# Kernel tuning notes

Hardware: AMD Instinct MI355X
Metric: run time of the kernel (lower is better)

Reference implementation:

```python
import jax, jax.numpy as jnp
import numpy as np

D = 128      # d_feat / d_model
L = 512      # seq_len
H = 8        # heads (hardcoded in FourierBlock weights)
E = D // H   # head dim = 16
MODES = 64   # low-frequency modes (mode_select='low' -> index = range(MODES))
MA = 25      # moving_avg kernel
NL = 2       # e_layers
DFF = 512
EPS = 1e-5


def _positional(length, dim):
    pos = jnp.arange(length, dtype=jnp.float32)[:, None]
    div = jnp.exp(jnp.arange(0, dim, 2, dtype=jnp.float32) * (-np.log(10000.0) / dim))
    pe = jnp.zeros((length, dim), dtype=jnp.float32)
    pe = pe.at[:, 0::2].set(jnp.sin(pos * div))
    pe = pe.at[:, 1::2].set(jnp.cos(pos * div))
    return pe


def _mov_mean(x, k):
    # series_decomp moving average: replicate-pad (k-1)//2 each side, window mean stride 1
    pad = (k - 1) // 2
    xp = jnp.concatenate([jnp.repeat(x[:, :1], pad, axis=1), x,
                          jnp.repeat(x[:, -1:], pad, axis=1)], axis=1)
    cs = jnp.cumsum(xp, axis=1)
    cs = jnp.concatenate([jnp.zeros_like(cs[:, :1]), cs], axis=1)
    return (cs[:, k:] - cs[:, :-k]) / k


def _fourier_layer(x, Wq, bq, Wo, bo, fwr, fwi):
    # AutoCorrelationLayer(query proj -> FourierBlock -> out proj); k/v projections are unused by FourierBlock
    B = x.shape[0]
    q = (x @ Wq + bq).reshape(B, L, H, E).transpose(0, 2, 3, 1)   # B,H,E,L
    xft = jnp.fft.rfft(q, axis=-1)                                # B,H,E,L//2+1
    Wc = fwr + 1j * fwi                                           # H,E,E,M (complex mode weights)
    sel = jnp.einsum('bhem,heom->bhom', xft[..., :MODES], Wc)
    out_ft = jnp.zeros((B, H, E, L // 2 + 1), dtype=sel.dtype).at[..., :MODES].set(sel)
    y = jnp.fft.irfft(out_ft, n=L, axis=-1)                       # B,H,E,L
    y = y.reshape(B, L, H * E)  # matches torch .view(B, L, -1) on contiguous B,H,E,L
    return y @ Wo + bo


def _enc_layer(x, Wq, bq, Wo, bo, fwr, fwi, W1, W2):
    x = x + _fourier_layer(x, Wq, bq, Wo, bo, fwr, fwi)
    x = x - _mov_mean(x, MA)                                  # decomp1 seasonal part
    y = jax.nn.gelu(x @ W1, approximate=False) @ W2           # 1x1 convs == matmuls, no bias
    s = x + y
    return s - _mov_mean(s, MA)                               # decomp2 seasonal part


def setup_inputs() -> dict:
    key = jax.random.key(0)
    ks = jax.random.split(key, 12)
    B = 128
    scale = 1.0 / (D * D)
    return {
        "x_enc": jax.random.normal(ks[0], (B, D * L), dtype=jnp.float32),
        "x_mark_enc": jax.random.uniform(ks[1], (B, D * L), dtype=jnp.float32),
        "x_dec": jnp.zeros((1,), jnp.float32),
        "x_mark_dec": jnp.zeros((1,), jnp.float32),
        "conv_w": jax.random.normal(ks[2], (D, D, 3), dtype=jnp.float32) * 0.02,
        "Wq": jax.random.normal(ks[3], (NL, D, D), dtype=jnp.float32) * 0.02,
        "bq": jnp.zeros((NL, D), jnp.float32),
        "Wo": jax.random.normal(ks[4], (NL, D, D), dtype=jnp.float32) * 0.02,
        "bo": jnp.zeros((NL, D), jnp.float32),
        "fwr": jax.random.uniform(ks[5], (NL, H, E, E, MODES), dtype=jnp.float32) * scale,
        "fwi": jax.random.uniform(ks[6], (NL, H, E, E, MODES), dtype=jnp.float32) * scale,
        "W1": jax.random.normal(ks[7], (NL, D, DFF), dtype=jnp.float32) * 0.02,
        "W2": jax.random.normal(ks[8], (NL, DFF, D), dtype=jnp.float32) * 0.02,
        "ln_g": jnp.ones((D,), jnp.float32),
        "ln_b": jnp.zeros((D,), jnp.float32),
        "proj_w": jax.random.normal(ks[9], (D * L,), dtype=jnp.float32) * 0.002,
        "proj_b": jnp.zeros((), jnp.float32),
    }


def reference(x_enc, x_mark_enc, x_dec, x_mark_dec, conv_w, Wq, bq, Wo, bo,
              fwr, fwi, W1, W2, ln_g, ln_b, proj_w, proj_b):
    B = x_enc.shape[0]
    x = x_enc.reshape(B, D, L).transpose(0, 2, 1)          # B,L,D
    mark = x_mark_enc.reshape(B, D, L).transpose(0, 2, 1)  # B,L,D
    # TokenEmbedding: Conv1d kernel 3, circular padding, no bias
    xc = x.transpose(0, 2, 1)                              # B,D,L
    xp = jnp.concatenate([xc[:, :, -1:], xc, xc[:, :, :1]], axis=-1)
    tok = jax.lax.conv_general_dilated(xp, conv_w, (1,), 'VALID',
                                       dimension_numbers=('NCH', 'OIH', 'NCH'))
    h = tok.transpose(0, 2, 1) + _positional(L, D)[None]   # + sinusoidal PE (dropout=0)
    for l in range(NL):
        h = _enc_layer(h, Wq[l], bq[l], Wo[l], bo[l], fwr[l], fwi[l], W1[l], W2[l])
    # my_Layernorm: LayerNorm over features, then subtract mean over time axis
    mu = h.mean(-1, keepdims=True)
    var = h.var(-1, keepdims=True)
    hn = (h - mu) / jnp.sqrt(var + EPS) * ln_g + ln_b
    hn = hn - hn.mean(axis=1, keepdims=True)
    o = jax.nn.gelu(hn, approximate=False) * mark          # act + mask-mul
    return o.reshape(B, -1) @ proj_w + proj_b              # (B,) after squeeze
```

## Files before the change

### kernel.cpp

```cpp
#include <hip/hip_runtime.h>
#include <math.h>

#define DFF 512
#define NLAYER 2
#define TS_LD 132

typedef __bf16 bf16x8 __attribute__((ext_vector_type(8)));
typedef __bf16 bf16x4 __attribute__((ext_vector_type(4)));
typedef float f32x4 __attribute__((ext_vector_type(4)));

__device__ __forceinline__ float4 f4_load(const float* p) { return *(const float4*)p; }
__device__ __forceinline__ void f4_store(float* p, float4 v) { *(float4*)p = v; }
__device__ __forceinline__ float4 f4_zero() { return make_float4(0.f, 0.f, 0.f, 0.f); }
__device__ __forceinline__ void f4_fma(float4& a, float s, const float4 w) {
    a.x += s * w.x; a.y += s * w.y; a.z += s * w.z; a.w += s * w.w;
}
__device__ __forceinline__ float gelu_f(float x) {
    return 0.5f * x * (1.0f + erff(x * 0.70710678118654752440f));
}
__device__ __forceinline__ void store_bf4(__bf16* p, float4 v) {
    __bf16 t[4] = {(__bf16)v.x, (__bf16)v.y, (__bf16)v.z, (__bf16)v.w};
    *(uint2*)p = *(uint2*)t;
}
__device__ __forceinline__ bf16x8 ld_b64x2(const __bf16* p) {
    bf16x4 lo = *(const bf16x4*)p;
    bf16x4 hi = *(const bf16x4*)(p + 4);
    return __builtin_shufflevector(lo, hi, 0, 1, 2, 3, 4, 5, 6, 7);
}

__global__ __launch_bounds__(256) void k_init(float* __restrict__ pe,
                                              __bf16* __restrict__ Fttb,
                                              __bf16* __restrict__ Gtb) {
    int idx = blockIdx.x * 256 + threadIdx.x;
    {
        int l = idx >> 7, d = idx & 127;
        int j = d >> 1;
        double div = exp((double)(2 * j) * (-log(10000.0) / 128.0));
        double a = (double)l * div;
        pe[idx] = (d & 1) ? (float)cos(a) : (float)sin(a);
    }
    {
        int m2 = idx >> 9, t = idx & 511;
        int m = m2 >> 1;
        int r = (m * t) & 511;
        double ang = (double)r * (6.283185307179586476925287 / 512.0);
        float cv = (float)cos(ang), sv = (float)sin(ang);
        float f = (m2 & 1) ? -sv : cv;
        Fttb[idx] = (__bf16)f;
        float s = (m == 0) ? (1.0f / 512.0f) : (2.0f / 512.0f);
        Gtb[t * 128 + m2] = (__bf16)(f * s);
    }
}

__global__ __launch_bounds__(256) void k_castw(const float* __restrict__ Wq,
                                               const float* __restrict__ Wo,
                                               const float* __restrict__ W1,
                                               const float* __restrict__ W2,
                                               const float* __restrict__ cw,
                                               __bf16* __restrict__ wbf,
                                               __bf16* __restrict__ cwtk) {
    int i = blockIdx.x * 256 + threadIdx.x;
    if (i < 65536) {
        int r = i & 16383, l = (i >> 14) & 1;
        int n = r >> 7, k = r & 127;
        const float* W = (i >= 32768) ? Wo : Wq;
        wbf[i] = (__bf16)W[l * 16384 + k * 128 + n];
    } else if (i < 196608) {
        int j = i - 65536;
        int l = j >> 16, r = j & 65535;
        int f = r >> 7, k = r & 127;
        wbf[i] = (__bf16)W1[l * 65536 + k * 512 + f];
    } else if (i < 327680) {
        int j = i - 196608;
        int l = j >> 16, r = j & 65535;
        int n = r >> 9, f = r & 511;
        wbf[i] = (__bf16)W2[l * 65536 + f * 128 + n];
    } else if (i < 376832) {
        int j = i - 327680;
        int s = j >> 14, r = j & 16383;
        int d = r >> 7, ii = r & 127;
        cwtk[j] = (__bf16)cw[(d * 128 + ii) * 3 + s];
    }
}

__global__ __launch_bounds__(256) void k_xpose(const float* __restrict__ xe,
                                               __bf16* __restrict__ xt) {
    __shared__ float ts[128][65];
    const int b = blockIdx.y, l0 = blockIdx.x * 64;
    for (int idx = threadIdx.x; idx < 128 * 16; idx += 256) {
        int d = idx >> 4, c4 = idx & 15;
        float4 v = f4_load(&xe[((size_t)b * 128 + d) * 512 + l0 + c4 * 4]);
        ts[d][c4 * 4 + 0] = v.x; ts[d][c4 * 4 + 1] = v.y;
        ts[d][c4 * 4 + 2] = v.z; ts[d][c4 * 4 + 3] = v.w;
    }
    __syncthreads();
#pragma unroll
    for (int p = 0; p < 4; ++p) {
        int l = (threadIdx.x >> 4) + p * 16;
        int d0 = (threadIdx.x & 15) * 8;
        __bf16 tmp[8];
#pragma unroll
        for (int j = 0; j < 8; ++j) tmp[j] = (__bf16)ts[d0 + j][l];
        *(uint4*)&xt[((size_t)b * 512 + l0 + l) * 128 + d0] = *(uint4*)tmp;
    }
}

__global__ __launch_bounds__(256) void k_embed_m(const __bf16* __restrict__ xt,
                                                 const __bf16* __restrict__ cwtk,
                                                 const float* __restrict__ pe,
                                                 float* __restrict__ h,
                                                 __bf16* __restrict__ hb) {
    __shared__ __align__(16) __bf16 xs[130 * 128];
    const int b = blockIdx.x >> 2, l0 = (blockIdx.x & 3) * 128;
    for (int c = threadIdx.x; c < 130 * 16; c += 256) {
        int r = c >> 4, g = c & 15;
        int gl = (l0 - 1 + r) & 511;
        *(uint4*)&xs[(r << 7) + ((g ^ (r & 7)) << 3)] =
            *(const uint4*)&xt[(((size_t)b * 512 + gl) << 7) + (g << 3)];
    }
    __syncthreads();
    const int lane = threadIdx.x & 63, wid = threadIdx.x >> 6;
    const int wrow = (wid & 1) * 64, wcol = (wid >> 1) * 64;
    const int m16 = lane & 15, quad = lane >> 4;
    f32x4 acc[4][4];
#pragma unroll
    for (int a = 0; a < 4; ++a)
#pragma unroll
        for (int bb = 0; bb < 4; ++bb) acc[a][bb] = {0.f, 0.f, 0.f, 0.f};
#pragma unroll
    for (int s = 0; s < 3; ++s) {
#pragma unroll
        for (int ks = 0; ks < 4; ++ks) {
            const int ko = ks * 32 + quad * 8;
            bf16x8 af[4], bfr[4];
#pragma unroll
            for (int rt = 0; rt < 4; ++rt) {
                int r = wrow + rt * 16 + m16 + s;
                af[rt] = *(const bf16x8*)&xs[(r << 7) + (((ks * 4 + quad) ^ (r & 7)) << 3)];
            }
#pragma unroll
            for (int ct = 0; ct < 4; ++ct)
                bfr[ct] = *(const bf16x8*)&cwtk[((size_t)(s * 128 + wcol + ct * 16 + m16) << 7) + ko];
#pragma unroll
            for (int rt = 0; rt < 4; ++rt)
#pragma unroll
                for (int ct = 0; ct < 4; ++ct)
                    acc[rt][ct] = __builtin_amdgcn_mfma_f32_16x16x32_bf16(
                        af[rt], bfr[ct], acc[rt][ct], 0, 0, 0);
        }
    }
#pragma unroll
    for (int ct = 0; ct < 4; ++ct) {
        int gcol = wcol + ct * 16 + m16;
#pragma unroll
        for (int rt = 0; rt < 4; ++rt)
#pragma unroll
            for (int r = 0; r < 4; ++r) {
                int l = l0 + wrow + rt * 16 + quad * 4 + r;
                float v = acc[rt][ct][r] + pe[l * 128 + gcol];
                size_t gi = (((size_t)b * 512 + l) << 7) + gcol;
                h[gi] = v;
                hb[gi] = (__bf16)v;
            }
    }
}

__global__ __launch_bounds__(256) void k_qprojT(const __bf16* __restrict__ Xb,
                                                const __bf16* __restrict__ Wt,
                                                const float* __restrict__ bias,
                                                __bf16* __restrict__ qT) {
    __shared__ __align__(16) __bf16 xs[128 * 128];
    const int rowBase = blockIdx.x * 128;
#pragma unroll
    for (int i = 0; i < 8; ++i) {
        int c = i * 256 + threadIdx.x;
        int r = c >> 4, g = c & 15;
        *(uint4*)&xs[(r << 7) + ((g ^ (r & 7)) << 3)] =
            *(const uint4*)&Xb[(((size_t)rowBase + r) << 7) + (g << 3)];
    }
    __syncthreads();
    const int lane = threadIdx.x & 63, wid = threadIdx.x >> 6;
    const int wn = (wid & 1) * 64, wr = (wid >> 1) * 64;
    const int m16 = lane & 15, quad = lane >> 4;
    f32x4 acc[4][4];
#pragma unroll
    for (int a = 0; a < 4; ++a)
#pragma unroll
        for (int b = 0; b < 4; ++b) acc[a][b] = {0.f, 0.f, 0.f, 0.f};
#pragma unroll
    for (int ks = 0; ks < 4; ++ks) {
        const int ko = ks * 32 + quad * 8;
        bf16x8 wf[4], xf[4];
#pragma unroll
        for (int rt = 0; rt < 4; ++rt)
            wf[rt] = *(const bf16x8*)&Wt[((size_t)(wn + rt * 16 + m16) << 7) + ko];
#pragma unroll
        for (int ct = 0; ct < 4; ++ct) {
            int r = wr + ct * 16 + m16;
            xf[ct] = *(const bf16x8*)&xs[(r << 7) + (((ks * 4 + quad) ^ (r & 7)) << 3)];
        }
#pragma unroll
        for (int rt = 0; rt < 4; ++rt)
#pragma unroll
            for (int ct = 0; ct < 4; ++ct)
                acc[rt][ct] = __builtin_amdgcn_mfma_f32_16x16x32_bf16(
                    wf[rt], xf[ct], acc[rt][ct], 0, 0, 0);
    }
#pragma unroll
    for (int rt = 0; rt < 4; ++rt)
#pragma unroll
        for (int r = 0; r < 4; ++r) {
            int n = wn + rt * 16 + quad * 4 + r;
            float bv = bias[n];
#pragma unroll
            for (int ct = 0; ct < 4; ++ct) {
                int grow = rowBase + wr + ct * 16 + m16;
                qT[(size_t)n * 65536 + grow] = (__bf16)(acc[rt][ct][r] + bv);
            }
        }
}

__global__ __launch_bounds__(128) void k_fdft_m(const __bf16* __restrict__ qT,
                                                const __bf16* __restrict__ Fttb,
                                                float* __restrict__ c) {
    const int b = blockIdx.y, d0 = blockIdx.x * 64;
    const int lane = threadIdx.x & 63, wid = threadIdx.x >> 6;
    const int wm = wid * 64;
    const int m16 = lane & 15, quad = lane >> 4;
    f32x4 acc[4][4];
#pragma unroll
    for (int a = 0; a < 4; ++a)
#pragma unroll
        for (int bb = 0; bb < 4; ++bb) acc[a][bb] = {0.f, 0.f, 0.f, 0.f};
    for (int ks = 0; ks < 16; ++ks) {
        const int ko = ks * 32 + quad * 8;
        bf16x8 af[4], bf[4];
#pragma unroll
        for (int rt = 0; rt < 4; ++rt)
            af[rt] = *(const bf16x8*)&qT[(size_t)(d0 + rt * 16 + m16) * 65536 + b * 512 + ko];
#pragma unroll
        for (int ct = 0; ct < 4; ++ct)
            bf[ct] = *(const bf16x8*)&Fttb[(size_t)(wm + ct * 16 + m16) * 512 + ko];
#pragma unroll
        for (int rt = 0; rt < 4; ++rt)
#pragma unroll
            for (int ct = 0; ct < 4; ++ct)
                acc[rt][ct] = __builtin_amdgcn_mfma_f32_16x16x32_bf16(
                    af[rt], bf[ct], acc[rt][ct], 0, 0, 0);
    }
#pragma unroll
    for (int ct = 0; ct < 4; ++ct) {
        int m2 = wm + ct * 16 + m16;
#pragma unroll
        for (int rt = 0; rt < 4; ++rt)
#pragma unroll
            for (int r = 0; r < 4; ++r) {
                int d = d0 + rt * 16 + quad * 4 + r;
                c[((size_t)b * 128 + d) * 128 + m2] = acc[rt][ct][r];
            }
    }
}

__global__ __launch_bounds__(256) void k_mix(const float* __restrict__ cbuf,
                                             const float* __restrict__ fwr,
                                             const float* __restrict__ fwi,
                                             __bf16* __restrict__ ddb) {
    __shared__ float cs[16][128];
    const int hh = blockIdx.x, b = blockIdx.y;
    for (int idx = threadIdx.x; idx < 16 * 32; idx += 256) {
        int e = idx >> 5, c4 = idx & 31;
        f4_store(&cs[e][c4 * 4],
                 f4_load(&cbuf[((size_t)b * 128 + hh * 16 + e) * 128 + c4 * 4]));
    }
    __syncthreads();
    const int m = threadIdx.x & 63, og = threadIdx.x >> 6;
    float dr[4] = {0.f, 0.f, 0.f, 0.f}, di[4] = {0.f, 0.f, 0.f, 0.f};
    for (int e = 0; e < 16; ++e) {
        float2 cv = *(const float2*)&cs[e][2 * m];
#pragma unroll
        for (int oi = 0; oi < 4; ++oi) {
            int o = og * 4 + oi;
            float wr = fwr[(((size_t)hh * 16 + e) * 16 + o) * 64 + m];
            float wi = fwi[(((size_t)hh * 16 + e) * 16 + o) * 64 + m];
            dr[oi] += cv.x * wr - cv.y * wi;
            di[oi] += cv.x * wi + cv.y * wr;
        }
    }
#pragma unroll
    for (int oi = 0; oi < 4; ++oi) {
        int o = og * 4 + oi;
        __bf16 t2[2] = {(__bf16)dr[oi], (__bf16)di[oi]};
        *(uint*)&ddb[((size_t)b * 128 + hh * 16 + o) * 128 + 2 * m] = *(uint*)t2;
    }
}

__global__ __launch_bounds__(256) void k_idft_m(const __bf16* __restrict__ ddb,
                                                const __bf16* __restrict__ Gtb,
                                                __bf16* __restrict__ y) {
    const int b = blockIdx.y, t0 = blockIdx.x * 128;
    const int lane = threadIdx.x & 63, wid = threadIdx.x >> 6;
    const int wt = (wid & 1) * 64, wh = (wid >> 1) * 64;
    const int m16 = lane & 15, quad = lane >> 4;
    f32x4 acc[4][4];
#pragma unroll
    for (int a = 0; a < 4; ++a)
#pragma unroll
        for (int bb = 0; bb < 4; ++bb) acc[a][bb] = {0.f, 0.f, 0.f, 0.f};
#pragma unroll
    for (int ks = 0; ks < 4; ++ks) {
        const int ko = ks * 32 + quad * 8;
        bf16x8 af[4], bf[4];
#pragma unroll
        for (int rt = 0; rt < 4; ++rt)
            af[rt] = *(const bf16x8*)&Gtb[(size_t)(t0 + wt + rt * 16 + m16) * 128 + ko];
#pragma unroll
        for (int ct = 0; ct < 4; ++ct)
            bf[ct] = *(const bf16x8*)&ddb[((size_t)b * 128 + wh + ct * 16 + m16) * 128 + ko];
#pragma unroll
        for (int rt = 0; rt < 4; ++rt)
#pragma unroll
            for (int ct = 0; ct < 4; ++ct)
                acc[rt][ct] = __builtin_amdgcn_mfma_f32_16x16x32_bf16(
                    af[rt], bf[ct], acc[rt][ct], 0, 0, 0);
    }
#pragma unroll
    for (int rt = 0; rt < 4; ++rt)
#pragma unroll
        for (int ct = 0; ct < 4; ++ct) {
            int ho = wh + ct * 16 + m16;
            int tb = t0 + wt + rt * 16 + quad * 4;
            __bf16 tmp[4] = {(__bf16)acc[rt][ct][0], (__bf16)acc[rt][ct][1],
                             (__bf16)acc[rt][ct][2], (__bf16)acc[rt][ct][3]};
            *(uint2*)&y[((size_t)b * 128 + ho) * 512 + tb] = *(uint2*)tmp;
        }
}

template <bool RES>
__global__ __launch_bounds__(256) void k_mgemm(const __bf16* __restrict__ Xb,
                                               const __bf16* __restrict__ Wt,
                                               const float* __restrict__ bias,
                                               const float* __restrict__ R,
                                               float* __restrict__ out) {
    __shared__ __align__(16) __bf16 xs[128 * 128];
    const int rowBase = blockIdx.x * 128;
#pragma unroll
    for (int i = 0; i < 8; ++i) {
        int c = i * 256 + threadIdx.x;
        int r = c >> 4, g = c & 15;
        *(uint4*)&xs[(r << 7) + ((g ^ (r & 7)) << 3)] =
            *(const uint4*)&Xb[(((size_t)rowBase + r) << 7) + (g << 3)];
    }
    __syncthreads();
    const int lane = threadIdx.x & 63, wid = threadIdx.x >> 6;
    const int wrow = (wid & 1) * 64, wcol = (wid >> 1) * 64;
    const int m16 = lane & 15, quad = lane >> 4;
    f32x4 acc[4][4];
#pragma unroll
    for (int a = 0; a < 4; ++a)
#pragma unroll
        for (int b = 0; b < 4; ++b) acc[a][b] = {0.f, 0.f, 0.f, 0.f};
#pragma unroll
    for (int ks = 0; ks < 4; ++ks) {
        const int ko = ks * 32 + quad * 8;
        const int xg = (((ks * 4 + quad) ^ (m16 & 7)) << 3);
        bf16x8 af[4], bfr[4];
#pragma unroll
        for (int rt = 0; rt < 4; ++rt)
            af[rt] = *(const bf16x8*)&xs[((wrow + rt * 16 + m16) << 7) + xg];
#pragma unroll
        for (int ct = 0; ct < 4; ++ct)
            bfr[ct] = *(const bf16x8*)&Wt[((size_t)(wcol + ct * 16 + m16) << 7) + ko];
#pragma unroll
        for (int rt = 0; rt < 4; ++rt)
#pragma unroll
            for (int ct = 0; ct < 4; ++ct)
                acc[rt][ct] = __builtin_amdgcn_mfma_f32_16x16x32_bf16(
                    af[rt], bfr[ct], acc[rt][ct], 0, 0, 0);
    }
#pragma unroll
    for (int ct = 0; ct < 4; ++ct) {
        int gcol = wcol + ct * 16 + m16;
        float bv = bias[gcol];
#pragma unroll
        for (int rt = 0; rt < 4; ++rt)
#pragma unroll
            for (int r = 0; r < 4; ++r) {
                size_t gi = ((size_t)(rowBase + wrow + rt * 16 + quad * 4 + r) << 7) + gcol;
                float v = acc[rt][ct][r] + bv;
                if (RES) v += R[gi];
                out[gi] = v;
            }
    }
}

__global__ __launch_bounds__(256) void k_ffnm(const __bf16* __restrict__ Xb,
                                              const float* __restrict__ Xf,
                                              const __bf16* __restrict__ W1t,
                                              const __bf16* __restrict__ W2t,
                                              float* __restrict__ out) {
    __shared__ __align__(16) __bf16 xs[128 * 128];
    __shared__ __align__(16) __bf16 ts[128 * TS_LD];
    const int rowBase = blockIdx.x * 128;
#pragma unroll
    for (int i = 0; i < 8; ++i) {
        int c = i * 256 + threadIdx.x;
        int r = c >> 4, g = c & 15;
        *(uint4*)&xs[(r << 7) + ((g ^ (r & 7)) << 3)] =
            *(const uint4*)&Xb[(((size_t)rowBase + r) << 7) + (g << 3)];
    }
    __syncthreads();
    const int lane = threadIdx.x & 63, wid = threadIdx.x >> 6;
    const int wrow = (wid & 1) * 64, wcol = (wid >> 1) * 64;
    const int m16 = lane & 15, quad = lane >> 4;
    f32x4 acc2[4][4];
#pragma unroll
    for (int a = 0; a < 4; ++a)
#pragma unroll
        for (int b = 0; b < 4; ++b) acc2[a][b] = {0.f, 0.f, 0.f, 0.f};

    for (int f0 = 0; f0 < DFF; f0 += 128) {
        f32x4 c1[4][4];
#pragma unroll
        for (int a = 0; a < 4; ++a)
#pragma unroll
            for (int b = 0; b < 4; ++b) c1[a][b] = {0.f, 0.f, 0.f, 0.f};
#pragma unroll
        for (int ks = 0; ks < 4; ++ks) {
            const int ko = ks * 32 + quad * 8;
            const int xg = (((ks * 4 + quad) ^ (m16 & 7)) << 3);
            bf16x8 af[4], bfr[4];
#pragma unroll
            for (int rt = 0; rt < 4; ++rt)
                af[rt] = *(const bf16x8*)&xs[((wrow + rt * 16 + m16) << 7) + xg];
#pragma unroll
            for (int ct = 0; ct < 4; ++ct)
                bfr[ct] = *(const bf16x8*)&W1t[((size_t)(f0 + wcol + ct * 16 + m16) << 7) + ko];
#pragma unroll
            for (int rt = 0; rt < 4; ++rt)
#pragma unroll
                for (int ct = 0; ct < 4; ++ct)
                    c1[rt][ct] = __builtin_amdgcn_mfma_f32_16x16x32_bf16(
                        af[rt], bfr[ct], c1[rt][ct], 0, 0, 0);
        }
#pragma unroll
        for (int rt = 0; rt < 4; ++rt)
#pragma unroll
            for (int ct = 0; ct < 4; ++ct)
#pragma unroll
                for (int r = 0; r < 4; ++r) {
                    int lrow = wrow + rt * 16 + quad * 4 + r;
                    int lcol = wcol + ct * 16 + m16;
                    ts[lrow * TS_LD + lcol] = (__bf16)gelu_f(c1[rt][ct][r]);
                }
        __syncthreads();
#pragma unroll
        for (int ks = 0; ks < 4; ++ks) {
            const int ko = ks * 32 + quad * 8;
            bf16x8 af[4], bfr[4];
#pragma unroll
            for (int rt = 0; rt < 4; ++rt)
                af[rt] = ld_b64x2(&ts[(wrow + rt * 16 + m16) * TS_LD + ko]);
#pragma unroll
            for (int ct = 0; ct < 4; ++ct)
                bfr[ct] = *(const bf16x8*)&W2t[((size_t)(wcol + ct * 16 + m16) << 9) + f0 + ko];
#pragma unroll
            for (int rt = 0; rt < 4; ++rt)
#pragma unroll
                for (int ct = 0; ct < 4; ++ct)
                    acc2[rt][ct] = __builtin_amdgcn_mfma_f32_16x16x32_bf16(
                        af[rt], bfr[ct], acc2[rt][ct], 0, 0, 0);
        }
        __syncthreads();
    }
#pragma unroll
    for (int ct = 0; ct < 4; ++ct) {
        int gcol = wcol + ct * 16 + m16;
#pragma unroll
        for (int rt = 0; rt < 4; ++rt)
#pragma unroll
            for (int r = 0; r < 4; ++r) {
                size_t gi = ((size_t)(rowBase + wrow + rt * 16 + quad * 4 + r) << 7) + gcol;
                out[gi] = acc2[rt][ct][r] + Xf[gi];
            }
    }
}

__global__ __launch_bounds__(256) void k_decomp(const float* __restrict__ X,
                                                float* __restrict__ out,
                                                __bf16* __restrict__ outb) {
    __shared__ float xs[88][128];
    const int b = blockIdx.y, l0 = blockIdx.x * 64;
    for (int idx = threadIdx.x; idx < 88 * 32; idx += 256) {
        int r = idx >> 5, c4 = idx & 31;
        int gl = l0 - 12 + r;
        gl = gl < 0 ? 0 : (gl > 511 ? 511 : gl);
        f4_store(&xs[r][c4 * 4], f4_load(&X[((size_t)b * 512 + gl) * 128 + c4 * 4]));
    }
    __syncthreads();
    const int dg = threadIdx.x & 31, lg = threadIdx.x >> 5;
    const int d0 = dg * 4, base = lg * 8;
    float4 s = f4_zero();
#pragma unroll
    for (int w = 0; w < 25; ++w) {
        float4 v = f4_load(&xs[base + w][d0]);
        s.x += v.x; s.y += v.y; s.z += v.z; s.w += v.w;
    }
    const float inv = 1.0f / 25.0f;
#pragma unroll
    for (int i = 0; i < 8; ++i) {
        int t = base + 12 + i;
        float4 x = f4_load(&xs[t][d0]);
        float4 o = make_float4(x.x - s.x * inv, x.y - s.y * inv,
                               x.z - s.z * inv, x.w - s.w * inv);
        size_t gi = ((size_t)b * 512 + l0 + lg * 8 + i) * 128 + d0;
        f4_store(&out[gi], o);
        store_bf4(&outb[gi], o);
        if (i < 7) {
            float4 a = f4_load(&xs[base + 25 + i][d0]);
            float4 r = f4_load(&xs[base + i][d0]);
            s.x += a.x - r.x; s.y += a.y - r.y; s.z += a.z - r.z; s.w += a.w - r.w;
        }
    }
}

__global__ __launch_bounds__(256) void k_ln(const float* __restrict__ X,
                                            const float* __restrict__ g,
                                            const float* __restrict__ bb,
                                            float* __restrict__ out) {
    const int row = blockIdx.x * 4 + (threadIdx.x >> 6);
    const int lane = threadIdx.x & 63;
    float2 v = *(const float2*)&X[(size_t)row * 128 + lane * 2];
    float s = v.x + v.y, ss = v.x * v.x + v.y * v.y;
#pragma unroll
    for (int o = 32; o; o >>= 1) {
        s += __shfl_xor(s, o);
        ss += __shfl_xor(ss, o);
    }
    float mu = s * (1.0f / 128.0f);
    float var = ss * (1.0f / 128.0f) - mu * mu;
    float rstd = rsqrtf(var + 1e-5f);
    float2 gg = *(const float2*)&g[lane * 2];
    float2 bv = *(const float2*)&bb[lane * 2];
    float2 o;
    o.x = (v.x - mu) * rstd * gg.x + bv.x;
    o.y = (v.y - mu) * rstd * gg.y + bv.y;
    *(float2*)&out[(size_t)row * 128 + lane * 2] = o;
}

__global__ __launch_bounds__(128) void k_colmean(const float* __restrict__ X,
                                                 float* __restrict__ cm) {
    const int b = blockIdx.y, l0 = blockIdx.x * 64, d = threadIdx.x;
    float s = 0.f;
    for (int l = l0; l < l0 + 64; ++l) s += X[((size_t)b * 512 + l) * 128 + d];
    atomicAdd(&cm[b * 128 + d], s);
}

__global__ __launch_bounds__(128) void k_final(const float* __restrict__ hn,
                                               const float* __restrict__ cm,
                                               const float* __restrict__ mark,
                                               const float* __restrict__ pw,
                                               const float* __restrict__ pb,
                                               float* __restrict__ out) {
    const int b = blockIdx.y, l0 = blockIdx.x * 128, d = threadIdx.x;
    const float c = cm[b * 128 + d] * (1.0f / 512.0f);
    float acc = 0.f;
    for (int l = l0; l < l0 + 128; ++l) {
        float v = hn[((size_t)b * 512 + l) * 128 + d] - c;
        acc += gelu_f(v) * mark[((size_t)b * 128 + d) * 512 + l] * pw[l * 128 + d];
    }
    __shared__ float red[2];
#pragma unroll
    for (int o = 32; o; o >>= 1) acc += __shfl_xor(acc, o);
    if ((threadIdx.x & 63) == 0) red[threadIdx.x >> 6] = acc;
    __syncthreads();
    if (threadIdx.x == 0) {
        float tot = red[0] + red[1];
        if (blockIdx.x == 0) tot += pb[0];
        atomicAdd(&out[b], tot);
    }
}

extern "C" void kernel_launch(void* const* d_in, const int* in_sizes, int n_in,
                              void* d_out, int out_size, void* d_ws, size_t ws_size,
                              hipStream_t stream) {
    const float* xe   = (const float*)d_in[0];
    const float* mark = (const float*)d_in[1];
    const float* cw   = (const float*)d_in[4];
    const float* Wq   = (const float*)d_in[5];
    const float* bq   = (const float*)d_in[6];
    const float* Wo   = (const float*)d_in[7];
    const float* bo   = (const float*)d_in[8];
    const float* fwr  = (const float*)d_in[9];
    const float* fwi  = (const float*)d_in[10];
    const float* W1   = (const float*)d_in[11];
    const float* W2   = (const float*)d_in[12];
    const float* lng  = (const float*)d_in[13];
    const float* lnb  = (const float*)d_in[14];
    const float* pw   = (const float*)d_in[15];
    const float* pb   = (const float*)d_in[16];
    float* out = (float*)d_out;

    float* ws    = (float*)d_ws;
    __bf16* Fttb = (__bf16*)ws;
    __bf16* Gtb  = (__bf16*)(ws + 65536);
    float* h     = ws + 131072;
    float* bufA  = ws + 8519680;
    __bf16* hb   = (__bf16*)(ws + 16908288);
    float* yrg   = ws + 21102592;
    float* cm    = ws + 25296896;
    __bf16* wbf  = (__bf16*)(ws + 25313280);
    float* pe    = yrg;
    __bf16* cwtk = (__bf16*)(yrg + 65536);
    float* cbuf  = yrg;
    __bf16* yb   = (__bf16*)yrg;
    __bf16* xt   = (__bf16*)bufA;
    __bf16* qT   = (__bf16*)bufA;
    __bf16* ddb  = (__bf16*)(bufA + 4194304);
    __bf16* Wqt  = wbf;
    __bf16* Wot  = wbf + 32768;
    __bf16* W1t  = wbf + 65536;
    __bf16* W2t  = wbf + 196608;

    k_init<<<256, 256, 0, stream>>>(pe, Fttb, Gtb);
    k_castw<<<1472, 256, 0, stream>>>(Wq, Wo, W1, W2, cw, wbf, cwtk);
    k_xpose<<<dim3(8, 128), 256, 0, stream>>>(xe, xt);
    k_embed_m<<<512, 256, 0, stream>>>(xt, cwtk, pe, h, hb);
    for (int l = 0; l < NLAYER; ++l) {
        k_qprojT<<<512, 256, 0, stream>>>(hb, Wqt + l * 16384, bq + l * 128, qT);
        k_fdft_m<<<dim3(2, 128), 128, 0, stream>>>(qT, Fttb, cbuf);
        k_mix<<<dim3(8, 128), 256, 0, stream>>>(cbuf, fwr + l * 131072,
                                                fwi + l * 131072, ddb);
        k_idft_m<<<dim3(4, 128), 256, 0, stream>>>(ddb, Gtb, yb);
        k_mgemm<true><<<512, 256, 0, stream>>>(yb, Wot + l * 16384, bo + l * 128,
                                               h, bufA);
        k_decomp<<<dim3(8, 128), 256, 0, stream>>>(bufA, h, hb);
        k_ffnm<<<512, 256, 0, stream>>>(hb, h, W1t + l * 65536, W2t + l * 65536, bufA);
        k_decomp<<<dim3(8, 128), 256, 0, stream>>>(bufA, h, hb);
    }
    k_ln<<<16384, 256, 0, stream>>>(h, lng, lnb, bufA);
    hipMemsetAsync(cm, 0, 16384 * sizeof(float), stream);
    k_colmean<<<dim3(8, 128), 128, 0, stream>>>(bufA, cm);
    hipMemsetAsync(d_out, 0, 128 * sizeof(float), stream);
    k_final<<<dim3(4, 128), 128, 0, stream>>>(bufA, cm, mark, pw, pb, out);

    (void)in_sizes; (void)n_in; (void)out_size; (void)ws_size;
}
```

Baseline: 658.5 us.

## Fuse forward DFT with mode mixing, drop LDS staging in GEMMs, retile decomp

Merges the forward-DFT MFMA kernel and the complex mode-mixing kernel into one kernel, with a 32-row DFT tile kept in LDS. This removes the float intermediate buffer round trip and one launch. Separately, the embed, qproj, mgemm and ffn kernels now read MFMA A/B fragments straight from global memory instead of staging them in swizzled LDS, which cuts LDS use and a barrier but relies on cache for reuse. The decomp kernel is retiled to 128 rows by 64 columns, which reduces the halo overhead per block.

```diff
diff --git a/kernel.cpp b/kernel.cpp
--- a/kernel.cpp
+++ b/kernel.cpp
@@ -4,6 +4,7 @@
 #define DFF 512
 #define NLAYER 2
 #define TS_LD 132
+#define CS_LD 130
 
 typedef __bf16 bf16x8 __attribute__((ext_vector_type(8)));
 typedef __bf16 bf16x4 __attribute__((ext_vector_type(4)));
@@ -12,9 +13,6 @@
 __device__ __forceinline__ float4 f4_load(const float* p) { return *(const float4*)p; }
 __device__ __forceinline__ void f4_store(float* p, float4 v) { *(float4*)p = v; }
 __device__ __forceinline__ float4 f4_zero() { return make_float4(0.f, 0.f, 0.f, 0.f); }
-__device__ __forceinline__ void f4_fma(float4& a, float s, const float4 w) {
-    a.x += s * w.x; a.y += s * w.y; a.z += s * w.z; a.w += s * w.w;
-}
 __device__ __forceinline__ float gelu_f(float x) {
     return 0.5f * x * (1.0f + erff(x * 0.70710678118654752440f));
 }
@@ -110,15 +108,7 @@
                                                  const float* __restrict__ pe,
                                                  float* __restrict__ h,
                                                  __bf16* __restrict__ hb) {
-    __shared__ __align__(16) __bf16 xs[130 * 128];
     const int b = blockIdx.x >> 2, l0 = (blockIdx.x & 3) * 128;
-    for (int c = threadIdx.x; c < 130 * 16; c += 256) {
-        int r = c >> 4, g = c & 15;
-        int gl = (l0 - 1 + r) & 511;
-        *(uint4*)&xs[(r << 7) + ((g ^ (r & 7)) << 3)] =
-            *(const uint4*)&xt[(((size_t)b * 512 + gl) << 7) + (g << 3)];
-    }
-    __syncthreads();
     const int lane = threadIdx.x & 63, wid = threadIdx.x >> 6;
     const int wrow = (wid & 1) * 64, wcol = (wid >> 1) * 64;
     const int m16 = lane & 15, quad = lane >> 4;
@@ -135,8 +125,8 @@
             bf16x8 af[4], bfr[4];
 #pragma unroll
             for (int rt = 0; rt < 4; ++rt) {
-                int r = wrow + rt * 16 + m16 + s;
-                af[rt] = *(const bf16x8*)&xs[(r << 7) + (((ks * 4 + quad) ^ (r & 7)) << 3)];
+                int gl = (l0 + wrow + rt * 16 + m16 + s - 1) & 511;
+                af[rt] = *(const bf16x8*)&xt[(((size_t)b * 512 + gl) << 7) + ko];
             }
 #pragma unroll
             for (int ct = 0; ct < 4; ++ct)
@@ -169,16 +159,7 @@
                                                 const __bf16* __restrict__ Wt,
                                                 const float* __restrict__ bias,
                                                 __bf16* __restrict__ qT) {
-    __shared__ __align__(16) __bf16 xs[128 * 128];
     const int rowBase = blockIdx.x * 128;
-#pragma unroll
-    for (int i = 0; i < 8; ++i) {
-        int c = i * 256 + threadIdx.x;
-        int r = c >> 4, g = c & 15;
-        *(uint4*)&xs[(r << 7) + ((g ^ (r & 7)) << 3)] =
-            *(const uint4*)&Xb[(((size_t)rowBase + r) << 7) + (g << 3)];
-    }
-    __syncthreads();
     const int lane = threadIdx.x & 63, wid = threadIdx.x >> 6;
     const int wn = (wid & 1) * 64, wr = (wid >> 1) * 64;
     const int m16 = lane & 15, quad = lane >> 4;
@@ -195,10 +176,8 @@
         for (int rt = 0; rt < 4; ++rt)
             wf[rt] = *(const bf16x8*)&Wt[((size_t)(wn + rt * 16 + m16) << 7) + ko];
 #pragma unroll
-        for (int ct = 0; ct < 4; ++ct) {
-            int r = wr + ct * 16 + m16;
-            xf[ct] = *(const bf16x8*)&xs[(r << 7) + (((ks * 4 + quad) ^ (r & 7)) << 3)];
-        }
+        for (int ct = 0; ct < 4; ++ct)
+            xf[ct] = *(const bf16x8*)&Xb[((size_t)(rowBase + wr + ct * 16 + m16) << 7) + ko];
 #pragma unroll
         for (int rt = 0; rt < 4; ++rt)
 #pragma unroll
@@ -220,77 +199,64 @@
         }
 }
 
-__global__ __launch_bounds__(128) void k_fdft_m(const __bf16* __restrict__ qT,
-                                                const __bf16* __restrict__ Fttb,
-                                                float* __restrict__ c) {
-    const int b = blockIdx.y, d0 = blockIdx.x * 64;
+__global__ __launch_bounds__(128) void k_fdftmix(const __bf16* __restrict__ qT,
+                                                 const __bf16* __restrict__ Fttb,
+                                                 const float* __restrict__ fwr,
+                                                 const float* __restrict__ fwi,
+                                                 __bf16* __restrict__ ddb) {
+    __shared__ float cs[32][CS_LD];
+    const int b = blockIdx.y, d0 = blockIdx.x * 32;
     const int lane = threadIdx.x & 63, wid = threadIdx.x >> 6;
     const int wm = wid * 64;
     const int m16 = lane & 15, quad = lane >> 4;
-    f32x4 acc[4][4];
-#pragma unroll
-    for (int a = 0; a < 4; ++a)
+    f32x4 acc[2][4];
+#pragma unroll
+    for (int a = 0; a < 2; ++a)
 #pragma unroll
         for (int bb = 0; bb < 4; ++bb) acc[a][bb] = {0.f, 0.f, 0.f, 0.f};
     for (int ks = 0; ks < 16; ++ks) {
         const int ko = ks * 32 + quad * 8;
-        bf16x8 af[4], bf[4];
-#pragma unroll
-        for (int rt = 0; rt < 4; ++rt)
+        bf16x8 af[2], bf[4];
+#pragma unroll
+        for (int rt = 0; rt < 2; ++rt)
             af[rt] = *(const bf16x8*)&qT[(size_t)(d0 + rt * 16 + m16) * 65536 + b * 512 + ko];
 #pragma unroll
         for (int ct = 0; ct < 4; ++ct)
             bf[ct] = *(const bf16x8*)&Fttb[(size_t)(wm + ct * 16 + m16) * 512 + ko];
 #pragma unroll
-        for (int rt = 0; rt < 4; ++rt)
+        for (int rt = 0; rt < 2; ++rt)
 #pragma unroll
             for (int ct = 0; ct < 4; ++ct)
                 acc[rt][ct] = __builtin_amdgcn_mfma_f32_16x16x32_bf16(
                     af[rt], bf[ct], acc[rt][ct], 0, 0, 0);
     }
 #pragma unroll
-    for (int ct = 0; ct < 4; ++ct) {
-        int m2 = wm + ct * 16 + m16;
-#pragma unroll
-        for (int rt = 0; rt < 4; ++rt)
-#pragma unroll
-            for (int r = 0; r < 4; ++r) {
-                int d = d0 + rt * 16 + quad * 4 + r;
-                c[((size_t)b * 128 + d) * 128 + m2] = acc[rt][ct][r];
-            }
-    }
-}
-
-__global__ __launch_bounds__(256) void k_mix(const float* __restrict__ cbuf,
-                                             const float* __restrict__ fwr,
-                                             const float* __restrict__ fwi,
-                                             __bf16* __restrict__ ddb) {
-    __shared__ float cs[16][128];
-    const int hh = blockIdx.x, b = blockIdx.y;
-    for (int idx = threadIdx.x; idx < 16 * 32; idx += 256) {
-        int e = idx >> 5, c4 = idx & 31;
-        f4_store(&cs[e][c4 * 4],
-                 f4_load(&cbuf[((size_t)b * 128 + hh * 16 + e) * 128 + c4 * 4]));
-    }
+    for (int rt = 0; rt < 2; ++rt)
+#pragma unroll
+        for (int ct = 0; ct < 4; ++ct)
+#pragma unroll
+            for (int r = 0; r < 4; ++r)
+                cs[rt * 16 + quad * 4 + r][wm + ct * 16 + m16] = acc[rt][ct][r];
     __syncthreads();
     const int m = threadIdx.x & 63, og = threadIdx.x >> 6;
-    float dr[4] = {0.f, 0.f, 0.f, 0.f}, di[4] = {0.f, 0.f, 0.f, 0.f};
-    for (int e = 0; e < 16; ++e) {
-        float2 cv = *(const float2*)&cs[e][2 * m];
-#pragma unroll
-        for (int oi = 0; oi < 4; ++oi) {
-            int o = og * 4 + oi;
-            float wr = fwr[(((size_t)hh * 16 + e) * 16 + o) * 64 + m];
-            float wi = fwi[(((size_t)hh * 16 + e) * 16 + o) * 64 + m];
-            dr[oi] += cv.x * wr - cv.y * wi;
-            di[oi] += cv.x * wi + cv.y * wr;
-        }
-    }
-#pragma unroll
-    for (int oi = 0; oi < 4; ++oi) {
-        int o = og * 4 + oi;
-        __bf16 t2[2] = {(__bf16)dr[oi], (__bf16)di[oi]};
-        *(uint*)&ddb[((size_t)b * 128 + hh * 16 + o) * 128 + 2 * m] = *(uint*)t2;
+#pragma unroll
+    for (int lh = 0; lh < 2; ++lh) {
+        int hh = (d0 >> 4) + lh;
+#pragma unroll
+        for (int oi = 0; oi < 8; ++oi) {
+            int o = og * 8 + oi;
+            float dr = 0.f, di = 0.f;
+#pragma unroll
+            for (int e = 0; e < 16; ++e) {
+                float2 cv = *(const float2*)&cs[lh * 16 + e][2 * m];
+                float wr = fwr[(((size_t)hh * 16 + e) * 16 + o) * 64 + m];
+                float wi = fwi[(((size_t)hh * 16 + e) * 16 + o) * 64 + m];
+                dr += cv.x * wr - cv.y * wi;
+                di += cv.x * wi + cv.y * wr;
+            }
+            __bf16 t2[2] = {(__bf16)dr, (__bf16)di};
+            *(uint*)&ddb[((size_t)b * 128 + hh * 16 + o) * 128 + 2 * m] = *(uint*)t2;
+        }
     }
 }
 
@@ -341,16 +307,7 @@
                                                const float* __restrict__ bias,
                                                const float* __restrict__ R,
                                                float* __restrict__ out) {
-    __shared__ __align__(16) __bf16 xs[128 * 128];
     const int rowBase = blockIdx.x * 128;
-#pragma unroll
-    for (int i = 0; i < 8; ++i) {
-        int c = i * 256 + threadIdx.x;
-        int r = c >> 4, g = c & 15;
-        *(uint4*)&xs[(r << 7) + ((g ^ (r & 7)) << 3)] =
-            *(const uint4*)&Xb[(((size_t)rowBase + r) << 7) + (g << 3)];
-    }
-    __syncthreads();
     const int lane = threadIdx.x & 63, wid = threadIdx.x >> 6;
     const int wrow = (wid & 1) * 64, wcol = (wid >> 1) * 64;
     const int m16 = lane & 15, quad = lane >> 4;
@@ -362,11 +319,10 @@
 #pragma unroll
     for (int ks = 0; ks < 4; ++ks) {
         const int ko = ks * 32 + quad * 8;
-        const int xg = (((ks * 4 + quad) ^ (m16 & 7)) << 3);
         bf16x8 af[4], bfr[4];
 #pragma unroll
         for (int rt = 0; rt < 4; ++rt)
-            af[rt] = *(const bf16x8*)&xs[((wrow + rt * 16 + m16) << 7) + xg];
+            af[rt] = *(const bf16x8*)&Xb[((size_t)(rowBase + wrow + rt * 16 + m16) << 7) + ko];
 #pragma unroll
         for (int ct = 0; ct < 4; ++ct)
             bfr[ct] = *(const bf16x8*)&Wt[((size_t)(wcol + ct * 16 + m16) << 7) + ko];
@@ -398,17 +354,8 @@
                                               const __bf16* __restrict__ W1t,
                                               const __bf16* __restrict__ W2t,
                                               float* __restrict__ out) {
-    __shared__ __align__(16) __bf16 xs[128 * 128];
     __shared__ __align__(16) __bf16 ts[128 * TS_LD];
     const int rowBase = blockIdx.x * 128;
-#pragma unroll
-    for (int i = 0; i < 8; ++i) {
-        int c = i * 256 + threadIdx.x;
-        int r = c >> 4, g = c & 15;
-        *(uint4*)&xs[(r << 7) + ((g ^ (r & 7)) << 3)] =
-            *(const uint4*)&Xb[(((size_t)rowBase + r) << 7) + (g << 3)];
-    }
-    __syncthreads();
     const int lane = threadIdx.x & 63, wid = threadIdx.x >> 6;
     const int wrow = (wid & 1) * 64, wcol = (wid >> 1) * 64;
     const int m16 = lane & 15, quad = lane >> 4;
@@ -427,11 +374,10 @@
 #pragma unroll
         for (int ks = 0; ks < 4; ++ks) {
             const int ko = ks * 32 + quad * 8;
-            const int xg = (((ks * 4 + quad) ^ (m16 & 7)) << 3);
             bf16x8 af[4], bfr[4];
 #pragma unroll
             for (int rt = 0; rt < 4; ++rt)
-                af[rt] = *(const bf16x8*)&xs[((wrow + rt * 16 + m16) << 7) + xg];
+                af[rt] = *(const bf16x8*)&Xb[((size_t)(rowBase + wrow + rt * 16 + m16) << 7) + ko];
 #pragma unroll
             for (int ct = 0; ct < 4; ++ct)
                 bfr[ct] = *(const bf16x8*)&W1t[((size_t)(f0 + wcol + ct * 16 + m16) << 7) + ko];
@@ -488,16 +434,18 @@
 __global__ __launch_bounds__(256) void k_decomp(const float* __restrict__ X,
                                                 float* __restrict__ out,
                                                 __bf16* __restrict__ outb) {
-    __shared__ float xs[88][128];
-    const int b = blockIdx.y, l0 = blockIdx.x * 64;
-    for (int idx = threadIdx.x; idx < 88 * 32; idx += 256) {
-        int r = idx >> 5, c4 = idx & 31;
+    __shared__ float xs[152][64];
+    const int b = blockIdx.y;
+    const int l0 = (blockIdx.x >> 1) * 128, dh = (blockIdx.x & 1) * 64;
+    for (int idx = threadIdx.x; idx < 152 * 16; idx += 256) {
+        int r = idx >> 4, c4 = idx & 15;
         int gl = l0 - 12 + r;
         gl = gl < 0 ? 0 : (gl > 511 ? 511 : gl);
-        f4_store(&xs[r][c4 * 4], f4_load(&X[((size_t)b * 512 + gl) * 128 + c4 * 4]));
+        f4_store(&xs[r][c4 * 4],
+                 f4_load(&X[((size_t)b * 512 + gl) * 128 + dh + c4 * 4]));
     }
     __syncthreads();
-    const int dg = threadIdx.x & 31, lg = threadIdx.x >> 5;
+    const int dg = threadIdx.x & 15, lg = threadIdx.x >> 4;
     const int d0 = dg * 4, base = lg * 8;
     float4 s = f4_zero();
 #pragma unroll
@@ -512,7 +460,7 @@
         float4 x = f4_load(&xs[t][d0]);
         float4 o = make_float4(x.x - s.x * inv, x.y - s.y * inv,
                                x.z - s.z * inv, x.w - s.w * inv);
-        size_t gi = ((size_t)b * 512 + l0 + lg * 8 + i) * 128 + d0;
+        size_t gi = ((size_t)b * 512 + l0 + lg * 8 + i) * 128 + dh + d0;
         f4_store(&out[gi], o);
         store_bf4(&outb[gi], o);
         if (i < 7) {
@@ -611,7 +559,6 @@
     __bf16* wbf  = (__bf16*)(ws + 25313280);
     float* pe    = yrg;
     __bf16* cwtk = (__bf16*)(yrg + 65536);
-    float* cbuf  = yrg;
     __bf16* yb   = (__bf16*)yrg;
     __bf16* xt   = (__bf16*)bufA;
     __bf16* qT   = (__bf16*)bufA;
@@ -627,9 +574,8 @@
     k_embed_m<<<512, 256, 0, stream>>>(xt, cwtk, pe, h, hb);
     for (int l = 0; l < NLAYER; ++l) {
         k_qprojT<<<512, 256, 0, stream>>>(hb, Wqt + l * 16384, bq + l * 128, qT);
-        k_fdft_m<<<dim3(2, 128), 128, 0, stream>>>(qT, Fttb, cbuf);
-        k_mix<<<dim3(8, 128), 256, 0, stream>>>(cbuf, fwr + l * 131072,
-                                                fwi + l * 131072, ddb);
+        k_fdftmix<<<dim3(4, 128), 128, 0, stream>>>(qT, Fttb, fwr + l * 131072,
+                                                    fwi + l * 131072, ddb);
         k_idft_m<<<dim3(4, 128), 256, 0, stream>>>(ddb, Gtb, yb);
         k_mgemm<true><<<512, 256, 0, stream>>>(yb, Wot + l * 16384, bo + l * 128,
                                                h, bufA);
```

Result: slower. 674.9 us (+2.5%).
